# Kernel tuning notes

Hardware: AMD Instinct MI355X
Metric: run time of the kernel (lower is better)

## Reference

```python
import jax, jax.numpy as jnp
import numpy as np

N = 50000      # nodes
F = 128        # in_channels
H = 4          # heads
C = 32         # out_channels per head
E = 800000     # edges (before self-loops)
NEG_SLOPE = 0.2


def setup_inputs() -> dict:
    key = jax.random.key(0)
    ks = jax.random.split(key, 10)
    x = jax.random.normal(ks[0], (N, F), dtype=jnp.float32)
    edge_index = jax.random.randint(ks[1], (2, E), 0, N, dtype=jnp.int32)
    s = 1.0 / np.sqrt(F)
    Wl = jax.random.uniform(ks[2], (H * C, F), jnp.float32, -s, s)
    bl = jax.random.uniform(ks[3], (H * C,), jnp.float32, -s, s)
    Wr = jax.random.uniform(ks[4], (H * C, F), jnp.float32, -s, s)
    br = jax.random.uniform(ks[5], (H * C,), jnp.float32, -s, s)
    Ws = jax.random.uniform(ks[6], (H * C, F), jnp.float32, -s, s)
    bs = jax.random.uniform(ks[7], (H * C,), jnp.float32, -s, s)
    att = jax.random.normal(ks[8], (H, C), jnp.float32) * (1.0 / np.sqrt(C))
    bias = jnp.zeros((H * C,), jnp.float32)
    return {"x": x, "edge_index": edge_index, "Wl": Wl, "bl": bl,
            "Wr": Wr, "br": br, "Ws": Ws, "bs": bs, "att": att, "bias": bias}


def reference(x, edge_index, Wl, bl, Wr, br, Ws, bs, att, bias):
    # add self loops (add_self_loops=True, edge_dim=None)
    loop = jnp.arange(N, dtype=edge_index.dtype)
    src = jnp.concatenate([edge_index[0], loop])  # j (source / neighbor)
    dst = jnp.concatenate([edge_index[1], loop])  # i (target, softmax segment)

    xl = (x @ Wl.T + bl).reshape(N, H, C)  # attention source transform (lin_l = lin_lAP)
    xr = (x @ Wr.T + br).reshape(N, H, C)  # attention target transform (lin_r = lin_rAP)
    xs = (x @ Ws.T + bs).reshape(N, H, C)  # aggregation transform (lin_s, linAggrSharing=False)

    # GATv2 edge score: a^T LeakyReLU(Theta_l x_j + Theta_r x_i)
    e = jax.nn.leaky_relu(xl[src] + xr[dst], NEG_SLOPE)      # [E+N, H, C]
    score = jnp.einsum('ehc,hc->eh', e, att)                 # [E+N, H]

    # segment softmax over incoming edges of each target node
    m = jax.ops.segment_max(score, dst, num_segments=N)      # [N, H]
    p = jnp.exp(score - m[dst])
    denom = jax.ops.segment_sum(p, dst, num_segments=N)      # [N, H]
    alpha = p / denom[dst]                                   # [E+N, H]

    # weighted scatter-add aggregation of lin_s-transformed sources
    out = jax.ops.segment_sum(xs[src] * alpha[..., None], dst, num_segments=N)
    return out.reshape(N, H * C) + bias                      # concat=True
```

## Files before the change

### kernel.cpp

```cpp
#include <hip/hip_runtime.h>
#include <hip/hip_bf16.h>

#define GN 50000
#define GF 128
#define GH 4
#define GC 32
#define GE 800000
#define GETOT (GE + GN)
#define HC 128
#define NEG 0.2f

#define TBLK ((GN + 63) / 64)
#define SBLK ((GETOT + 255) / 256)
#define LDSW 132

typedef __bf16 bf16x8 __attribute__((ext_vector_type(8)));
typedef float  f32x4  __attribute__((ext_vector_type(4)));
typedef unsigned short ushort8 __attribute__((ext_vector_type(8)));

__device__ __forceinline__ uint f32_to_bf16_rne(float f) {
    unsigned u = __float_as_uint(f);
    return (u + 0x7fffu + ((u >> 16) & 1u)) >> 16;
}

__device__ __forceinline__ bf16x8 cvt8(const float* p) {
    float4 v0 = *(const float4*)p;
    float4 v1 = *(const float4*)(p + 4);
    ushort8 o;
    o[0] = (ushort)f32_to_bf16_rne(v0.x); o[1] = (ushort)f32_to_bf16_rne(v0.y);
    o[2] = (ushort)f32_to_bf16_rne(v0.z); o[3] = (ushort)f32_to_bf16_rne(v0.w);
    o[4] = (ushort)f32_to_bf16_rne(v1.x); o[5] = (ushort)f32_to_bf16_rne(v1.y);
    o[6] = (ushort)f32_to_bf16_rne(v1.z); o[7] = (ushort)f32_to_bf16_rne(v1.w);
    return __builtin_bit_cast(bf16x8, o);
}

template<int CTRL>
__device__ __forceinline__ float dpp_add(float v) {
    int s = __builtin_bit_cast(int, v);
    int y = __builtin_amdgcn_update_dpp(s, s, CTRL, 0xF, 0xF, false);
    return v + __builtin_bit_cast(float, y);
}

__global__ __launch_bounds__(256) void conv_w(
    const float* __restrict__ Wl, const float* __restrict__ Wr,
    const float* __restrict__ Ws, ushort* __restrict__ Wb,
    int* __restrict__ deg)
{
    int idx = blockIdx.x * 256 + threadIdx.x;
    if (idx < 3 * GF * GF / 8) {
        int m = idx / 2048;
        int e = (idx - m * 2048) * 8;
        const float* W = (m == 0) ? Wl : (m == 1) ? Wr : Ws;
        float4 v0 = *(const float4*)&W[e];
        float4 v1 = *(const float4*)&W[e + 4];
        ushort8 o;
        o[0] = (ushort)f32_to_bf16_rne(v0.x); o[1] = (ushort)f32_to_bf16_rne(v0.y);
        o[2] = (ushort)f32_to_bf16_rne(v0.z); o[3] = (ushort)f32_to_bf16_rne(v0.w);
        o[4] = (ushort)f32_to_bf16_rne(v1.x); o[5] = (ushort)f32_to_bf16_rne(v1.y);
        o[6] = (ushort)f32_to_bf16_rne(v1.z); o[7] = (ushort)f32_to_bf16_rne(v1.w);
        *(ushort8*)&Wb[m * 16384 + e] = o;
    }
    int z = idx - 6144;
    if (z >= 0 && z < GN / 4)
        *(int4*)&deg[z * 4] = make_int4(0, 0, 0, 0);
}

__global__ __launch_bounds__(256) void fused_transform_slot(
    const float* __restrict__ x, const ushort* __restrict__ Wb,
    const float* __restrict__ bl, const float* __restrict__ br,
    const float* __restrict__ bs,
    const int* __restrict__ ei, int* __restrict__ deg, int* __restrict__ slot,
    uint* __restrict__ xi, float* __restrict__ xr)
{
    __shared__ float lds_f[64 * LDSW];

    if (blockIdx.x >= TBLK) {
        int e = (blockIdx.x - TBLK) * 256 + threadIdx.x;
        if (e < GETOT) {
            int dst = (e < GE) ? ei[GE + e] : (e - GE);
            slot[e] = atomicAdd(&deg[dst], 1);
        }
        return;
    }

    const int bx    = blockIdx.x;
    const int tid   = threadIdx.x;
    const int wave  = tid >> 6;
    const int lane  = tid & 63;
    const int colb  = lane & 15;
    const int klane = lane >> 4;
    const int row0  = bx * 64 + wave * 16;

    bf16x8 a[4];
    {
        int rA = row0 + colb;
        const float* ap = x + (size_t)min(rA, GN - 1) * GF + klane * 8;
#pragma unroll
        for (int kb = 0; kb < 4; ++kb)
            a[kb] = cvt8(ap + kb * 32);
    }

    const int woff = colb * GF + klane * 8;
    uint* lds_u = (uint*)lds_f;

    f32x4 acc0[8], acc2[8];
#pragma unroll
    for (int n = 0; n < 8; ++n) {
        acc0[n] = (f32x4){0.f, 0.f, 0.f, 0.f};
        acc2[n] = (f32x4){0.f, 0.f, 0.f, 0.f};
    }
#pragma unroll
    for (int kb = 0; kb < 4; ++kb) {
        const ushort* w0 = Wb + woff + kb * 32;
        const ushort* w2 = Wb + 2 * 16384 + woff + kb * 32;
#pragma unroll
        for (int n = 0; n < 8; ++n) {
            bf16x8 b0 = *(const bf16x8*)(w0 + n * 2048);
            bf16x8 b2 = *(const bf16x8*)(w2 + n * 2048);
            acc0[n] = __builtin_amdgcn_mfma_f32_16x16x32_bf16(a[kb], b0, acc0[n], 0, 0, 0);
            acc2[n] = __builtin_amdgcn_mfma_f32_16x16x32_bf16(a[kb], b2, acc2[n], 0, 0, 0);
        }
    }
#pragma unroll
    for (int n = 0; n < 8; ++n) {
        int col = n * 16 + colb;
        float blv = bl[col], bsv = bs[col];
#pragma unroll
        for (int r = 0; r < 4; ++r) {
            int rl = wave * 16 + klane * 4 + r;
            uint w = f32_to_bf16_rne(acc0[n][r] + blv)
                   | (f32_to_bf16_rne(acc2[n][r] + bsv) << 16);
            lds_u[rl * LDSW + col] = w;
        }
    }
    __syncthreads();
#pragma unroll
    for (int i = 0; i < 8; ++i) {
        int c = i * 256 + tid;
        int row = c >> 5, cin = c & 31;
        if (bx * 64 + row < GN) {
            uint4 v = *(uint4*)&lds_u[row * LDSW + cin * 4];
            *(uint4*)&xi[((size_t)(bx * 64 + row)) * 128 + cin * 4] = v;
        }
    }
    __syncthreads();

    f32x4 acc1[8];
#pragma unroll
    for (int n = 0; n < 8; ++n) acc1[n] = (f32x4){0.f, 0.f, 0.f, 0.f};
#pragma unroll
    for (int kb = 0; kb < 4; ++kb) {
        const ushort* w1 = Wb + 16384 + woff + kb * 32;
#pragma unroll
        for (int n = 0; n < 8; ++n) {
            bf16x8 b1 = *(const bf16x8*)(w1 + n * 2048);
            acc1[n] = __builtin_amdgcn_mfma_f32_16x16x32_bf16(a[kb], b1, acc1[n], 0, 0, 0);
        }
    }
#pragma unroll
    for (int n = 0; n < 8; ++n) {
        int col = n * 16 + colb;
        float bv = br[col];
#pragma unroll
        for (int r = 0; r < 4; ++r) {
            int rl = wave * 16 + klane * 4 + r;
            lds_f[rl * LDSW + col] = acc1[n][r] + bv;
        }
    }
    __syncthreads();
#pragma unroll
    for (int i = 0; i < 8; ++i) {
        int c = i * 256 + tid;
        int row = c >> 5, cin = c & 31;
        if (bx * 64 + row < GN) {
            float4 v = *(float4*)&lds_f[row * LDSW + cin * 4];
            *(float4*)&xr[((size_t)(bx * 64 + row)) * 128 + cin * 4] = v;
        }
    }
}

__global__ __launch_bounds__(1024) void scan_kernel(const int* __restrict__ deg,
                                                    int* __restrict__ rowstart)
{
    __shared__ int sums[1024];
    const int t = threadIdx.x;
    const int CH = 52;
    const int start = t * CH;
    const int end = min(start + CH, GN);

    int s = 0;
    if (start + CH <= GN) {
#pragma unroll
        for (int g = 0; g < 13; ++g) {
            int4 v = *(const int4*)&deg[start + g * 4];
            s += v.x + v.y + v.z + v.w;
        }
    } else {
        for (int i = start; i < end; ++i) s += deg[i];
    }
    sums[t] = s;
    __syncthreads();
    for (int off = 1; off < 1024; off <<= 1) {
        int v = (t >= off) ? sums[t - off] : 0;
        __syncthreads();
        sums[t] += v;
        __syncthreads();
    }
    int run = sums[t] - s;
    if (start + CH <= GN) {
#pragma unroll
        for (int g = 0; g < 13; ++g) {
            int4 v = *(const int4*)&deg[start + g * 4];
            int4 w;
            w.x = run;
            w.y = run + v.x;
            w.z = run + v.x + v.y;
            w.w = run + v.x + v.y + v.z;
            run += v.x + v.y + v.z + v.w;
            *(int4*)&rowstart[start + g * 4] = w;
        }
    } else {
        for (int i = start; i < end; ++i) { rowstart[i] = run; run += deg[i]; }
    }
    if (t == 1023) rowstart[GN] = run;
}

__global__ void scatter_kernel(const int* __restrict__ ei,
                               const int* __restrict__ rowstart,
                               const int* __restrict__ slot,
                               int* __restrict__ csr_src)
{
    int e = blockIdx.x * 256 + threadIdx.x;
    if (e >= GETOT) return;
    int src, dst;
    if (e < GE) { src = ei[e]; dst = ei[GE + e]; }
    else        { src = dst = e - GE; }
    csr_src[rowstart[dst] + slot[e]] = src;
}

__device__ __forceinline__ void edge_acc(uint2 xv, float2 xr2, float2 at2,
                                         bool live, float& denom,
                                         float& ax, float& ay)
{
    float zx = __uint_as_float((xv.x & 0xffffu) << 16) + xr2.x;
    float zy = __uint_as_float((xv.y & 0xffffu) << 16) + xr2.y;
    zx = (zx > 0.f) ? zx : NEG * zx;
    zy = (zy > 0.f) ? zy : NEG * zy;
    float sc = fmaf(zx, at2.x, zy * at2.y);
    sc = dpp_add<0xB1>(sc);
    sc = dpp_add<0x4E>(sc);
    sc = dpp_add<0x124>(sc);
    sc = dpp_add<0x128>(sc);
    float pe = live ? __expf(sc) : 0.f;
    denom += pe;
    ax = fmaf(pe, __uint_as_float(xv.x & 0xffff0000u), ax);
    ay = fmaf(pe, __uint_as_float(xv.y & 0xffff0000u), ay);
}

__global__ __launch_bounds__(256) void gat_kernel(
    const uint* __restrict__ xi, const float* __restrict__ xr,
    const float* __restrict__ att, const float* __restrict__ bias,
    const int* __restrict__ rowstart, const int* __restrict__ csr_src,
    float* __restrict__ out)
{
    const int wave = threadIdx.x >> 6;
    const int lane = threadIdx.x & 63;
    const int node = blockIdx.x * 4 + wave;
    const int l2 = lane * 2;

    const float2 xr2 = *(const float2*)&xr[(size_t)node * HC + l2];
    const float2 at2 = *(const float2*)&att[l2];
    const float2 bi2 = *(const float2*)&bias[l2];

    const int s0 = rowstart[node];
    const int s1 = rowstart[node + 1];

    float denom = 0.f, ax = 0.f, ay = 0.f;
    for (int base = s0; base < s1; base += 64) {
        int nsrc = (base + lane < s1) ? csr_src[base + lane] : 0;
        int cnt = min(64, s1 - base);
        for (int t = 0; t < cnt; t += 4) {
            int sA = __shfl(nsrc, t, 64);
            int sB = __shfl(nsrc, t + 1, 64);
            int sC = __shfl(nsrc, t + 2, 64);
            int sD = __shfl(nsrc, t + 3, 64);
            uint2 vA = *(const uint2*)&xi[(size_t)sA * 128 + l2];
            uint2 vB = *(const uint2*)&xi[(size_t)sB * 128 + l2];
            uint2 vC = *(const uint2*)&xi[(size_t)sC * 128 + l2];
            uint2 vD = *(const uint2*)&xi[(size_t)sD * 128 + l2];
            edge_acc(vA, xr2, at2, true,          denom, ax, ay);
            edge_acc(vB, xr2, at2, (t + 1 < cnt), denom, ax, ay);
            edge_acc(vC, xr2, at2, (t + 2 < cnt), denom, ax, ay);
            edge_acc(vD, xr2, at2, (t + 3 < cnt), denom, ax, ay);
        }
    }
    const float inv = 1.f / denom;
    float2 o;
    o.x = fmaf(ax, inv, bi2.x);
    o.y = fmaf(ay, inv, bi2.y);
    *(float2*)&out[(size_t)node * HC + l2] = o;
}

extern "C" void kernel_launch(void* const* d_in, const int* in_sizes, int n_in,
                              void* d_out, int out_size, void* d_ws, size_t ws_size,
                              hipStream_t stream)
{
    const float* x   = (const float*)d_in[0];
    const int*   ei  = (const int*)  d_in[1];
    const float* Wl  = (const float*)d_in[2];
    const float* bl  = (const float*)d_in[3];
    const float* Wr  = (const float*)d_in[4];
    const float* br  = (const float*)d_in[5];
    const float* Ws  = (const float*)d_in[6];
    const float* bs  = (const float*)d_in[7];
    const float* att = (const float*)d_in[8];
    const float* bias= (const float*)d_in[9];
    float* out = (float*)d_out;

    uint*   xi = (uint*)d_ws;
    ushort* Wb = (ushort*)(xi + (size_t)GN * 128);
    float*  xr = (float*)(Wb + 3 * GF * GF);
    int* deg      = (int*)(xr + (size_t)GN * HC);
    int* rowstart = deg + GN;
    int* slot     = rowstart + GN + 1;
    int* csr_src  = slot + GETOT;

    conv_w<<<(6144 + GN / 4 + 255) / 256, 256, 0, stream>>>(Wl, Wr, Ws, Wb, deg);

    fused_transform_slot<<<TBLK + SBLK, 256, 0, stream>>>(
        x, Wb, bl, br, bs, ei, deg, slot, xi, xr);

    scan_kernel<<<1, 1024, 0, stream>>>(deg, rowstart);

    scatter_kernel<<<SBLK, 256, 0, stream>>>(ei, rowstart, slot, csr_src);

    gat_kernel<<<GN / 4, 256, 0, stream>>>((const uint*)xi, xr, att, bias,
                                           rowstart, csr_src, out);
}
```

Baseline: 248.7 us.

## Interleave transform and slot blocks; unroll edge gather by eight

The fused transform/slot kernel now interleaves one GEMM transform block with four degree-counting atomic blocks across the grid, instead of placing all transform blocks first. This lets compute-heavy and atomic-heavy work share CUs concurrently. The aggregation loop also issues eight neighbor gathers per iteration instead of four, to put more loads in flight. The cost is higher register pressure and more wasted loads for short neighbor lists.

```diff
diff --git a/kernel.cpp b/kernel.cpp
--- a/kernel.cpp
+++ b/kernel.cpp
@@ -12,6 +12,7 @@
 
 #define TBLK ((GN + 63) / 64)
 #define SBLK ((GETOT + 255) / 256)
+#define INTR 5
 #define LDSW 132
 
 typedef __bf16 bf16x8 __attribute__((ext_vector_type(8)));
@@ -74,8 +75,19 @@
 {
     __shared__ float lds_f[64 * LDSW];
 
-    if (blockIdx.x >= TBLK) {
-        int e = (blockIdx.x - TBLK) * 256 + threadIdx.x;
+    const int b = blockIdx.x;
+    int bx;
+    bool is_transform;
+    int sb;
+    if (b < INTR * TBLK) {
+        if (b % INTR == 0) { is_transform = true;  bx = b / INTR; sb = 0; }
+        else               { is_transform = false; bx = 0; sb = b - (b / INTR + 1); }
+    } else {
+        is_transform = false; bx = 0; sb = b - TBLK;
+    }
+
+    if (!is_transform) {
+        int e = sb * 256 + threadIdx.x;
         if (e < GETOT) {
             int dst = (e < GE) ? ei[GE + e] : (e - GE);
             slot[e] = atomicAdd(&deg[dst], 1);
@@ -83,7 +95,6 @@
         return;
     }
 
-    const int bx    = blockIdx.x;
     const int tid   = threadIdx.x;
     const int wave  = tid >> 6;
     const int lane  = tid & 63;
@@ -279,19 +290,19 @@
     for (int base = s0; base < s1; base += 64) {
         int nsrc = (base + lane < s1) ? csr_src[base + lane] : 0;
         int cnt = min(64, s1 - base);
-        for (int t = 0; t < cnt; t += 4) {
-            int sA = __shfl(nsrc, t, 64);
-            int sB = __shfl(nsrc, t + 1, 64);
-            int sC = __shfl(nsrc, t + 2, 64);
-            int sD = __shfl(nsrc, t + 3, 64);
-            uint2 vA = *(const uint2*)&xi[(size_t)sA * 128 + l2];
-            uint2 vB = *(const uint2*)&xi[(size_t)sB * 128 + l2];
-            uint2 vC = *(const uint2*)&xi[(size_t)sC * 128 + l2];
-            uint2 vD = *(const uint2*)&xi[(size_t)sD * 128 + l2];
-            edge_acc(vA, xr2, at2, true,          denom, ax, ay);
-            edge_acc(vB, xr2, at2, (t + 1 < cnt), denom, ax, ay);
-            edge_acc(vC, xr2, at2, (t + 2 < cnt), denom, ax, ay);
-            edge_acc(vD, xr2, at2, (t + 3 < cnt), denom, ax, ay);
+        for (int t = 0; t < cnt; t += 8) {
+            int   se[8];
+            uint2 ve[8];
+#pragma unroll
+            for (int u = 0; u < 8; ++u)
+                se[u] = __shfl(nsrc, t + u, 64);
+#pragma unroll
+            for (int u = 0; u < 8; ++u)
+                ve[u] = *(const uint2*)&xi[(size_t)se[u] * 128 + l2];
+            edge_acc(ve[0], xr2, at2, true, denom, ax, ay);
+#pragma unroll
+            for (int u = 1; u < 8; ++u)
+                edge_acc(ve[u], xr2, at2, (t + u < cnt), denom, ax, ay);
         }
     }
     const float inv = 1.f / denom;
```

Measured after the change: 249.6 us. No clear change (+0.4%).
